# Kernel tuning notes

Hardware: AMD Instinct MI355X
Metric: run time of the kernel (lower is better)

## Reference

```python
import jax, jax.numpy as jnp
import numpy as np
from jax import lax

K = 10
ALPHA = 0.1
N_NODES = 100000
N_EDGES = 3200000


def setup_inputs() -> dict:
    key = jax.random.key(0)
    ks = jax.random.split(key, 6)
    x = jax.random.normal(ks[0], (N_NODES, 256), dtype=jnp.float32)
    edge_index = jax.random.randint(ks[1], (2, N_EDGES), 0, N_NODES, dtype=jnp.int64)
    w1 = jax.random.normal(ks[2], (256, 256), dtype=jnp.float32) * (1.0 / np.sqrt(256))
    b1 = jax.random.normal(ks[3], (256,), dtype=jnp.float32) * 0.01
    w2 = jax.random.normal(ks[4], (64, 256), dtype=jnp.float32) * (1.0 / np.sqrt(256))
    b2 = jax.random.normal(ks[5], (64,), dtype=jnp.float32) * 0.01
    return {"x": x, "edge_index": edge_index, "w1": w1, "b1": b1, "w2": w2, "b2": b2}


def reference(x, edge_index, w1, b1, w2, b2):
    # Eval mode: dropout is identity.
    h = jax.nn.relu(x @ w1.T + b1)          # [N, hidden]
    z = h @ w2.T + b2                        # [N, out]

    n = x.shape[0]
    loop = jnp.arange(n, dtype=edge_index.dtype)
    row = jnp.concatenate([edge_index[0], loop])   # sources (with self-loops)
    col = jnp.concatenate([edge_index[1], loop])   # targets (with self-loops)

    # gcn_norm: D^{-1/2} (A + I) D^{-1/2}, degree at target nodes
    deg = jax.ops.segment_sum(jnp.ones_like(col, dtype=z.dtype), col, num_segments=n)
    dinv = lax.rsqrt(deg)                    # deg >= 1 due to self-loops
    norm = dinv[row] * dinv[col]             # [E+N]

    x0 = z

    def step(xk, _):
        msg = xk[row] * norm[:, None]                          # gather + scale
        agg = jax.ops.segment_sum(msg, col, num_segments=n)    # scatter-add
        return (1.0 - ALPHA) * agg + ALPHA * x0, None

    out, _ = lax.scan(step, z, None, length=K)
    return out
```

## Files before the change

### kernel.cpp

```cpp
#include <hip/hip_runtime.h>
#include <hip/hip_bf16.h>


#define HIDDEN 256
#define OUTF   64
#define NB_BLK 256

typedef __attribute__((ext_vector_type(8))) unsigned short ushort8;
typedef __attribute__((ext_vector_type(8))) short short8v;
typedef __attribute__((ext_vector_type(4))) float f32x4;

__device__ inline float b2f(unsigned short u) {
    union { unsigned int i; float f; } c;
    c.i = ((unsigned int)u) << 16;
    return c.f;
}
__device__ inline unsigned short f2b(float f) {
    union { float f; unsigned int i; } c;
    c.f = f;
    unsigned int x = c.i;
    unsigned int r = (x + 0x7fff + ((x >> 16) & 1)) >> 16;
    return (unsigned short)r;
}
__device__ inline short8v cvt8v(float4 A, float4 B) {
    short8v o;
    o[0] = (short)f2b(A.x); o[1] = (short)f2b(A.y);
    o[2] = (short)f2b(A.z); o[3] = (short)f2b(A.w);
    o[4] = (short)f2b(B.x); o[5] = (short)f2b(B.y);
    o[6] = (short)f2b(B.z); o[7] = (short)f2b(B.w);
    return o;
}
__device__ inline short8v cvt8(const float* s) {
    return cvt8v(((const float4*)s)[0], ((const float4*)s)[1]);
}

__device__ inline bool detect_i64(const int* __restrict__ p) {
    int acc = 0;
#pragma unroll
    for (int i = 0; i < 16; ++i) acc |= p[2 * i + 1];
    return acc == 0;
}
__device__ inline int load_idx(const void* eiv, long long flat, bool is64) {
    if (is64) return (int)((const long long*)eiv)[flat];
    return ((const int*)eiv)[flat];
}

__global__ __launch_bounds__(256) void part_hist_kernel(const void* __restrict__ eiv,
                                                        long long E, int* __restrict__ bh,
                                                        int n, int nb) {
    __shared__ int hist[512];
    bool is64 = detect_i64((const int*)eiv);
    int t = threadIdx.x, b = blockIdx.x;
    for (int i = t; i < 512; i += 256) hist[i] = 0;
    __syncthreads();
    long long chunk = (E + NB_BLK - 1) / NB_BLK;
    long long beg = (long long)b * chunk, end = min(E, beg + chunk);
    for (long long e = beg + t; e < end; e += 256) {
        int c = load_idx(eiv, E + e, is64);
        if ((unsigned)c < (unsigned)n) atomicAdd(&hist[c >> 8], 1);
    }
    __syncthreads();
    for (int i = t; i < nb; i += 256) bh[i * NB_BLK + b] = hist[i];
}

__global__ __launch_bounds__(256) void part_colscan_kernel(const int* __restrict__ bh,
                                                           int* __restrict__ pre,
                                                           int* __restrict__ btot) {
    __shared__ int s[NB_BLK];
    int g = blockIdx.x, t = threadIdx.x;
    int v = bh[g * NB_BLK + t];
    s[t] = v;
    __syncthreads();
    for (int o = 1; o < NB_BLK; o <<= 1) {
        int tv = (t >= o) ? s[t - o] : 0;
        __syncthreads();
        s[t] += tv;
        __syncthreads();
    }
    pre[g * NB_BLK + t] = s[t] - v;
    if (t == NB_BLK - 1) btot[g] = s[t];
}

__global__ __launch_bounds__(512) void part_bscan_kernel(const int* __restrict__ btot,
                                                         int* __restrict__ bofs, int nb) {
    __shared__ int s[512];
    int t = threadIdx.x;
    int v = (t < nb) ? btot[t] : 0;
    s[t] = v;
    __syncthreads();
    for (int o = 1; o < 512; o <<= 1) {
        int tv = (t >= o) ? s[t - o] : 0;
        __syncthreads();
        s[t] += tv;
        __syncthreads();
    }
    if (t < nb) bofs[t] = s[t] - v;
    if (t == 511) bofs[nb] = s[511];
}

__global__ __launch_bounds__(256) void part_scatter_kernel(const void* __restrict__ eiv,
                                                           long long E,
                                                           const int* __restrict__ bofs,
                                                           const int* __restrict__ pre,
                                                           int2* __restrict__ pairs,
                                                           int n, int nb) {
    __shared__ int cur[512];
    bool is64 = detect_i64((const int*)eiv);
    int t = threadIdx.x, b = blockIdx.x;
    for (int i = t; i < nb; i += 256) cur[i] = bofs[i] + pre[i * NB_BLK + b];
    __syncthreads();
    long long chunk = (E + NB_BLK - 1) / NB_BLK;
    long long beg = (long long)b * chunk, end = min(E, beg + chunk);
    for (long long e = beg + t; e < end; e += 256) {
        int r = load_idx(eiv, e, is64);
        int c = load_idx(eiv, E + e, is64);
        if ((unsigned)c >= (unsigned)n || (unsigned)r >= (unsigned)n) continue;
        int pos = atomicAdd(&cur[c >> 8], 1);
        pairs[pos] = make_int2(c, r);
    }
}

__global__ __launch_bounds__(256) void csr_bucket_kernel(const int2* __restrict__ pairs,
                                                         const int* __restrict__ bofs,
                                                         int* __restrict__ ofs,
                                                         float* __restrict__ dinv,
                                                         int* __restrict__ csr_src,
                                                         int n, int nb) {
    __shared__ int hist[256];
    __shared__ int scn[256];
    int b = blockIdx.x;
    int t = threadIdx.x;
    int node0 = b << 8;
    int cnt = min(256, n - node0);

    hist[t] = 0;
    __syncthreads();
    int beg = bofs[b], end = bofs[b + 1];
    for (int e = beg + t; e < end; e += 256) atomicAdd(&hist[pairs[e].x & 255], 1);
    __syncthreads();
    int v = hist[t];
    scn[t] = v;
    __syncthreads();
    for (int o = 1; o < 256; o <<= 1) {
        int tv = (t >= o) ? scn[t - o] : 0;
        __syncthreads();
        scn[t] += tv;
        __syncthreads();
    }
    int excl = scn[t] - v;
    if (t < cnt) {
        ofs[node0 + t] = beg + excl;
        dinv[node0 + t] = rsqrtf((float)(v + 1));
    }
    if (b == nb - 1 && t == 0) ofs[n] = end;
    __syncthreads();
    hist[t] = beg + excl;
    __syncthreads();
    for (int e = beg + t; e < end; e += 256) {
        int2 p = pairs[e];
        int pos = atomicAdd(&hist[p.x & 255], 1);
        csr_src[pos] = p.y;
    }
}

__global__ __launch_bounds__(256) void pack_w_kernel(const float* __restrict__ w1,
                                                     const float* __restrict__ w2,
                                                     unsigned short* __restrict__ w1p,
                                                     unsigned short* __restrict__ w2p) {
    int id = blockIdx.x * 256 + threadIdx.x;
    if (id < 8192) {
        int ks = id >> 10, rem = id & 1023;
        int f = rem >> 2, kg = rem & 3;
        short8v o = cvt8(w1 + (size_t)f * HIDDEN + ks * 32 + kg * 8);
        *(short8v*)(w1p + ((size_t)(ks * 1024 + (f >> 4) * 64 + kg * 16 + (f & 15)) << 3)) = o;
    } else if (id < 8192 + 2048) {
        int q = id - 8192;
        int j = q >> 5, kslot = q & 31;
        short8v o = cvt8(w2 + (size_t)j * HIDDEN + kslot * 8);
        *(short8v*)(w2p +
                    ((size_t)((j >> 4) * 512 + (kslot >> 2) * 64 + (kslot & 3) * 16 + (j & 15))
                     << 3)) = o;
    }
}

__global__ __launch_bounds__(512) void mlp_mfma_kernel(const float* __restrict__ x,
                                                       const unsigned short* __restrict__ w1p,
                                                       const float* __restrict__ b1,
                                                       const unsigned short* __restrict__ w2p,
                                                       const float* __restrict__ b2,
                                                       const float* __restrict__ dinv,
                                                       unsigned short* __restrict__ xb0,
                                                       unsigned short* __restrict__ g0, int n) {
    __shared__ __align__(16) union {
        struct { unsigned short w1s[8192]; unsigned short xs[2048]; } p1;
        unsigned short h[64 * 264];
    } u;

    const int t = threadIdx.x;
    const int w = t >> 6;
    const int l = t & 63;
    const int c = l & 15, g = l >> 4;
    const int node0 = blockIdx.x * 64;

    const bool xrole = (t < 256);
    const int sm = t >> 2, skg = t & 3;
    const int snode = node0 + sm;
    const int wu0 = t - 256;
    const int xunit = ((sm >> 4) * 64 + skg * 16 + (sm & 15)) << 3;

    f32x4 acc[4][2];
#pragma unroll
    for (int a = 0; a < 4; ++a)
#pragma unroll
        for (int b = 0; b < 2; ++b) acc[a][b] = (f32x4)0.f;

    float4 pxa0 = make_float4(0.f, 0.f, 0.f, 0.f), pxb0 = pxa0;
    float4 pxa1 = pxa0, pxb1 = pxa0;
    short8v pw[4];

    auto loadx = [&](int ks, float4& A, float4& B) {
        if (snode < n) {
            const float4* xp = (const float4*)(x + (size_t)snode * HIDDEN + ks * 32 + skg * 8);
            A = xp[0];
            B = xp[1];
        }
    };
    auto loadw = [&](int ks) {
        const unsigned short* wsrc = w1p + (size_t)ks * 8192;
#pragma unroll
        for (int i = 0; i < 4; ++i)
            pw[i] = *(const short8v*)(wsrc + ((size_t)(wu0 + i * 256) << 3));
    };
    auto mfma_step = [&]() {
        short8v af[4], bf[2];
#pragma unroll
        for (int mt = 0; mt < 4; ++mt)
            af[mt] = *(const short8v*)&u.p1.xs[(mt * 64 + l) << 3];
#pragma unroll
        for (int j = 0; j < 2; ++j)
            bf[j] = *(const short8v*)&u.p1.w1s[((w * 2 + j) * 64 + l) << 3];
#pragma unroll
        for (int mt = 0; mt < 4; ++mt)
#pragma unroll
            for (int j = 0; j < 2; ++j)
                acc[mt][j] =
                    __builtin_amdgcn_mfma_f32_16x16x32_bf16(af[mt], bf[j], acc[mt][j], 0, 0, 0);
    };
    auto wwrite = [&]() {
#pragma unroll
        for (int i = 0; i < 4; ++i)
            *(short8v*)&u.p1.w1s[(wu0 + i * 256) << 3] = pw[i];
    };

    if (xrole) {
        loadx(0, pxa0, pxb0);
        loadx(1, pxa1, pxb1);
    } else {
        loadw(0);
    }

    for (int ks = 0; ks < 8; ks += 2) {
        if (xrole) *(short8v*)&u.p1.xs[xunit] = cvt8v(pxa0, pxb0);
        else wwrite();
        __syncthreads();
        if (xrole) {
            if (ks + 2 < 8) loadx(ks + 2, pxa0, pxb0);
        } else {
            loadw(ks + 1);
        }
        mfma_step();
        __syncthreads();
        if (xrole) *(short8v*)&u.p1.xs[xunit] = cvt8v(pxa1, pxb1);
        else wwrite();
        __syncthreads();
        if (xrole) {
            if (ks + 3 < 8) loadx(ks + 3, pxa1, pxb1);
        } else {
            if (ks + 2 < 8) loadw(ks + 2);
        }
        mfma_step();
        __syncthreads();
    }

#pragma unroll
    for (int j = 0; j < 2; ++j) {
        int col = w * 32 + j * 16 + c;
        float b1v = b1[col];
#pragma unroll
        for (int mt = 0; mt < 4; ++mt)
#pragma unroll
            for (int r = 0; r < 4; ++r) {
                int row = mt * 16 + g * 4 + r;
                u.h[row * 264 + col] = f2b(fmaxf(acc[mt][j][r] + b1v, 0.f));
            }
    }
    __syncthreads();

    const int rt = w >> 1;
    const int cb = (w & 1) * 2;
    f32x4 acc2[2];
#pragma unroll
    for (int j = 0; j < 2; ++j) acc2[j] = (f32x4)0.f;
#pragma unroll
    for (int ks = 0; ks < 8; ++ks) {
        short8v a2 = *(const short8v*)&u.h[(rt * 16 + c) * 264 + ks * 32 + g * 8];
#pragma unroll
        for (int j = 0; j < 2; ++j) {
            short8v bv = *(const short8v*)(w2p + ((size_t)((cb + j) * 512 + ks * 64 + l) << 3));
            acc2[j] = __builtin_amdgcn_mfma_f32_16x16x32_bf16(a2, bv, acc2[j], 0, 0, 0);
        }
    }
#pragma unroll
    for (int j = 0; j < 2; ++j) {
        int col = (cb + j) * 16 + c;
        float bb = b2[col];
#pragma unroll
        for (int r = 0; r < 4; ++r) {
            int node = node0 + rt * 16 + g * 4 + r;
            if (node < n) {
                float zv = acc2[j][r] + bb;
                float di = dinv[node];
                xb0[(size_t)node * OUTF + col] = f2b(0.1f * zv);
                g0[(size_t)node * OUTF + col] = f2b(di * zv);
            }
        }
    }
}

template <int LAST>
__global__ __launch_bounds__(256) void prop_kernel(const unsigned short* __restrict__ gk,
                                                   const unsigned short* __restrict__ xb0,
                                                   unsigned short* __restrict__ gn,
                                                   float* __restrict__ out,
                                                   const int* __restrict__ ofs,
                                                   const int* __restrict__ csr_src,
                                                   const float* __restrict__ dinv, int n) {
    int gid = blockIdx.x * 256 + threadIdx.x;
    int node = gid >> 5;
    int sub = gid & 31;
    int part = sub & 7;
    int q = sub >> 3;
    if (node >= n) return;

    int beg = ofs[node];
    int end = ofs[node + 1];
    int len = end - beg;
    int e0 = beg + ((len * q) >> 2);
    int e1 = beg + ((len * (q + 1)) >> 2);

    float acc[8];
#pragma unroll
    for (int j = 0; j < 8; ++j) acc[j] = 0.f;

    const size_t poff = (size_t)part * 8;
    int e = e0;
    for (; e + 3 < e1; e += 4) {
        int s0 = csr_src[e];
        int s1 = csr_src[e + 1];
        int s2 = csr_src[e + 2];
        int s3 = csr_src[e + 3];
        ushort8 a = *(const ushort8*)(gk + ((size_t)s0 << 6) + poff);
        ushort8 b = *(const ushort8*)(gk + ((size_t)s1 << 6) + poff);
        ushort8 cc = *(const ushort8*)(gk + ((size_t)s2 << 6) + poff);
        ushort8 d = *(const ushort8*)(gk + ((size_t)s3 << 6) + poff);
#pragma unroll
        for (int j = 0; j < 8; ++j) acc[j] += b2f(a[j]);
#pragma unroll
        for (int j = 0; j < 8; ++j) acc[j] += b2f(b[j]);
#pragma unroll
        for (int j = 0; j < 8; ++j) acc[j] += b2f(cc[j]);
#pragma unroll
        for (int j = 0; j < 8; ++j) acc[j] += b2f(d[j]);
    }
    for (; e < e1; ++e) {
        int s0 = csr_src[e];
        ushort8 a = *(const ushort8*)(gk + ((size_t)s0 << 6) + poff);
#pragma unroll
        for (int j = 0; j < 8; ++j) acc[j] += b2f(a[j]);
    }
    if (q == 0) {
        ushort8 a = *(const ushort8*)(gk + ((size_t)node << 6) + poff);
#pragma unroll
        for (int j = 0; j < 8; ++j) acc[j] += b2f(a[j]);
    }

#pragma unroll
    for (int j = 0; j < 8; ++j) acc[j] += __shfl_xor(acc[j], 8);
#pragma unroll
    for (int j = 0; j < 8; ++j) acc[j] += __shfl_xor(acc[j], 16);

    if (q != 0) return;

    float di = dinv[node];
    ushort8 xv = *(const ushort8*)(xb0 + ((size_t)node << 6) + poff);
    float res[8];
#pragma unroll
    for (int j = 0; j < 8; ++j) res[j] = 0.9f * di * acc[j] + b2f(xv[j]);

    if (LAST) {
        float4* o4 = (float4*)(out + (size_t)node * OUTF + poff);
        o4[0] = make_float4(res[0], res[1], res[2], res[3]);
        o4[1] = make_float4(res[4], res[5], res[6], res[7]);
    } else {
        ushort8 o;
#pragma unroll
        for (int j = 0; j < 8; ++j) o[j] = f2b(di * res[j]);
        *(ushort8*)(gn + ((size_t)node << 6) + poff) = o;
    }
}

extern "C" void kernel_launch(void* const* d_in, const int* in_sizes, int n_in,
                              void* d_out, int out_size, void* d_ws, size_t ws_size,
                              hipStream_t stream) {
    const float* x = (const float*)d_in[0];
    const void* ei = d_in[1];
    const float* w1 = (const float*)d_in[2];
    const float* b1 = (const float*)d_in[3];
    const float* w2 = (const float*)d_in[4];
    const float* b2 = (const float*)d_in[5];
    float* out = (float*)d_out;

    int n = in_sizes[0] / HIDDEN;
    long long E = (long long)in_sizes[1] / 2;
    int nb = (n + 255) >> 8;

    char* ws = (char*)d_ws;
    size_t off = 0;
    auto alloc = [&](size_t bytes) {
        void* p = ws + off;
        off += (bytes + 511) & ~(size_t)511;
        return p;
    };
    unsigned short* xb0 = (unsigned short*)alloc((size_t)n * OUTF * 2);
    size_t gmark = off;
    unsigned short* gA = (unsigned short*)alloc((size_t)n * OUTF * 2);
    unsigned short* gB = (unsigned short*)alloc((size_t)n * OUTF * 2);
    int2* pairs = (int2*)(ws + gmark);
    float* dinv = (float*)alloc((size_t)n * 4);
    int* ofs = (int*)alloc((size_t)(n + 1) * 4);
    int* csr_src = (int*)alloc((size_t)E * 4);
    int* bh = (int*)alloc((size_t)512 * NB_BLK * 4);
    int* pre = (int*)alloc((size_t)512 * NB_BLK * 4);
    int* btot = (int*)alloc(512 * 4);
    int* bofs = (int*)alloc(513 * 4);
    unsigned short* w1p = (unsigned short*)alloc(65536 * 2);
    unsigned short* w2p = (unsigned short*)alloc(16384 * 2);

    pack_w_kernel<<<40, 256, 0, stream>>>(w1, w2, w1p, w2p);

    part_hist_kernel<<<NB_BLK, 256, 0, stream>>>(ei, E, bh, n, nb);
    part_colscan_kernel<<<nb, NB_BLK, 0, stream>>>(bh, pre, btot);
    part_bscan_kernel<<<1, 512, 0, stream>>>(btot, bofs, nb);
    part_scatter_kernel<<<NB_BLK, 256, 0, stream>>>(ei, E, bofs, pre, pairs, n, nb);
    csr_bucket_kernel<<<nb, 256, 0, stream>>>(pairs, bofs, ofs, dinv, csr_src, n, nb);

    mlp_mfma_kernel<<<(n + 63) / 64, 512, 0, stream>>>(x, w1p, b1, w2p, b2, dinv, xb0, gA, n);

    int prop_blocks = (int)(((size_t)n * 32 + 255) / 256);
    for (int k = 0; k < 10; ++k) {
        const unsigned short* gin = (k & 1) ? gB : gA;
        unsigned short* gout = (k & 1) ? gA : gB;
        if (k == 9) {
            prop_kernel<1><<<prop_blocks, 256, 0, stream>>>(gin, xb0, nullptr, out, ofs,
                                                            csr_src, dinv, n);
        } else {
            prop_kernel<0><<<prop_blocks, 256, 0, stream>>>(gin, xb0, gout, nullptr, ofs,
                                                            csr_src, dinv, n);
        }
    }
}
```

Before: 681.4 us.

## Split features into two halves per XCD with dynamic chunk scheduling in propagation

```diff
diff --git a/kernel.cpp b/kernel.cpp
--- a/kernel.cpp
+++ b/kernel.cpp
@@ -102,7 +102,7 @@
                                                            long long E,
                                                            const int* __restrict__ bofs,
                                                            const int* __restrict__ pre,
-                                                           int2* __restrict__ pairs,
+                                                           unsigned int* __restrict__ pairs,
                                                            int n, int nb) {
     __shared__ int cur[512];
     bool is64 = detect_i64((const int*)eiv);
@@ -116,11 +116,11 @@
         int c = load_idx(eiv, E + e, is64);
         if ((unsigned)c >= (unsigned)n || (unsigned)r >= (unsigned)n) continue;
         int pos = atomicAdd(&cur[c >> 8], 1);
-        pairs[pos] = make_int2(c, r);
-    }
-}
-
-__global__ __launch_bounds__(256) void csr_bucket_kernel(const int2* __restrict__ pairs,
+        pairs[pos] = ((unsigned int)(c & 255) << 24) | (unsigned int)r;
+    }
+}
+
+__global__ __launch_bounds__(256) void csr_bucket_kernel(const unsigned int* __restrict__ pairs,
                                                          const int* __restrict__ bofs,
                                                          int* __restrict__ ofs,
                                                          float* __restrict__ dinv,
@@ -136,7 +136,7 @@
     hist[t] = 0;
     __syncthreads();
     int beg = bofs[b], end = bofs[b + 1];
-    for (int e = beg + t; e < end; e += 256) atomicAdd(&hist[pairs[e].x & 255], 1);
+    for (int e = beg + t; e < end; e += 256) atomicAdd(&hist[pairs[e] >> 24], 1);
     __syncthreads();
     int v = hist[t];
     scn[t] = v;
@@ -157,9 +157,9 @@
     hist[t] = beg + excl;
     __syncthreads();
     for (int e = beg + t; e < end; e += 256) {
-        int2 p = pairs[e];
-        int pos = atomicAdd(&hist[p.x & 255], 1);
-        csr_src[pos] = p.y;
+        unsigned int pr = pairs[e];
+        int pos = atomicAdd(&hist[pr >> 24], 1);
+        csr_src[pos] = (int)(pr & 0xFFFFFFu);
     }
 }
 
@@ -189,8 +189,10 @@
                                                        const unsigned short* __restrict__ w2p,
                                                        const float* __restrict__ b2,
                                                        const float* __restrict__ dinv,
-                                                       unsigned short* __restrict__ xb0,
-                                                       unsigned short* __restrict__ g0, int n) {
+                                                       unsigned short* __restrict__ xbh0,
+                                                       unsigned short* __restrict__ xbh1,
+                                                       unsigned short* __restrict__ g00,
+                                                       unsigned short* __restrict__ g01, int n) {
     __shared__ __align__(16) union {
         struct { unsigned short w1s[8192]; unsigned short xs[2048]; } p1;
         unsigned short h[64 * 264];
@@ -313,99 +315,111 @@
 #pragma unroll
     for (int j = 0; j < 2; ++j) {
         int col = (cb + j) * 16 + c;
+        int h2 = col >> 5;
+        int col32 = col & 31;
         float bb = b2[col];
+        unsigned short* xbp = h2 ? xbh1 : xbh0;
+        unsigned short* gp = h2 ? g01 : g00;
 #pragma unroll
         for (int r = 0; r < 4; ++r) {
             int node = node0 + rt * 16 + g * 4 + r;
             if (node < n) {
                 float zv = acc2[j][r] + bb;
                 float di = dinv[node];
-                xb0[(size_t)node * OUTF + col] = f2b(0.1f * zv);
-                g0[(size_t)node * OUTF + col] = f2b(di * zv);
+                size_t idx = ((size_t)node << 5) + col32;
+                xbp[idx] = f2b(0.1f * zv);
+                gp[idx] = f2b(di * zv);
             }
         }
     }
 }
 
 template <int LAST>
-__global__ __launch_bounds__(256) void prop_kernel(const unsigned short* __restrict__ gk,
-                                                   const unsigned short* __restrict__ xb0,
-                                                   unsigned short* __restrict__ gn,
+__global__ __launch_bounds__(256) void prop_kernel(const unsigned short* __restrict__ gi0,
+                                                   const unsigned short* __restrict__ gi1,
+                                                   const unsigned short* __restrict__ xbh0,
+                                                   const unsigned short* __restrict__ xbh1,
+                                                   unsigned short* __restrict__ go0,
+                                                   unsigned short* __restrict__ go1,
                                                    float* __restrict__ out,
                                                    const int* __restrict__ ofs,
                                                    const int* __restrict__ csr_src,
-                                                   const float* __restrict__ dinv, int n) {
-    int gid = blockIdx.x * 256 + threadIdx.x;
-    int node = gid >> 5;
-    int sub = gid & 31;
-    int part = sub & 7;
-    int q = sub >> 3;
-    if (node >= n) return;
-
-    int beg = ofs[node];
-    int end = ofs[node + 1];
-    int len = end - beg;
-    int e0 = beg + ((len * q) >> 2);
-    int e1 = beg + ((len * (q + 1)) >> 2);
-
-    float acc[8];
-#pragma unroll
-    for (int j = 0; j < 8; ++j) acc[j] = 0.f;
-
-    const size_t poff = (size_t)part * 8;
-    int e = e0;
-    for (; e + 3 < e1; e += 4) {
-        int s0 = csr_src[e];
-        int s1 = csr_src[e + 1];
-        int s2 = csr_src[e + 2];
-        int s3 = csr_src[e + 3];
-        ushort8 a = *(const ushort8*)(gk + ((size_t)s0 << 6) + poff);
-        ushort8 b = *(const ushort8*)(gk + ((size_t)s1 << 6) + poff);
-        ushort8 cc = *(const ushort8*)(gk + ((size_t)s2 << 6) + poff);
-        ushort8 d = *(const ushort8*)(gk + ((size_t)s3 << 6) + poff);
-#pragma unroll
-        for (int j = 0; j < 8; ++j) acc[j] += b2f(a[j]);
-#pragma unroll
-        for (int j = 0; j < 8; ++j) acc[j] += b2f(b[j]);
-#pragma unroll
-        for (int j = 0; j < 8; ++j) acc[j] += b2f(cc[j]);
-#pragma unroll
-        for (int j = 0; j < 8; ++j) acc[j] += b2f(d[j]);
-    }
-    for (; e < e1; ++e) {
-        int s0 = csr_src[e];
-        ushort8 a = *(const ushort8*)(gk + ((size_t)s0 << 6) + poff);
-#pragma unroll
-        for (int j = 0; j < 8; ++j) acc[j] += b2f(a[j]);
-    }
-    if (q == 0) {
-        ushort8 a = *(const ushort8*)(gk + ((size_t)node << 6) + poff);
-#pragma unroll
-        for (int j = 0; j < 8; ++j) acc[j] += b2f(a[j]);
-    }
-
-#pragma unroll
-    for (int j = 0; j < 8; ++j) acc[j] += __shfl_xor(acc[j], 8);
-#pragma unroll
-    for (int j = 0; j < 8; ++j) acc[j] += __shfl_xor(acc[j], 16);
-
-    if (q != 0) return;
-
-    float di = dinv[node];
-    ushort8 xv = *(const ushort8*)(xb0 + ((size_t)node << 6) + poff);
-    float res[8];
-#pragma unroll
-    for (int j = 0; j < 8; ++j) res[j] = 0.9f * di * acc[j] + b2f(xv[j]);
-
-    if (LAST) {
-        float4* o4 = (float4*)(out + (size_t)node * OUTF + poff);
-        o4[0] = make_float4(res[0], res[1], res[2], res[3]);
-        o4[1] = make_float4(res[4], res[5], res[6], res[7]);
-    } else {
-        ushort8 o;
-#pragma unroll
-        for (int j = 0; j < 8; ++j) o[j] = f2b(di * res[j]);
-        *(ushort8*)(gn + ((size_t)node << 6) + poff) = o;
+                                                   const float* __restrict__ dinv,
+                                                   int* __restrict__ cnt, int n) {
+    __shared__ int sc;
+    unsigned int xcd;
+    asm("s_getreg_b32 %0, hwreg(HW_REG_XCC_ID)" : "=s"(xcd));
+    const int t = threadIdx.x;
+    const int p = t & 3;
+    const int nl = t >> 2;
+    const int nchunks = (n + 63) >> 6;
+    const size_t poff = (size_t)p * 8;
+
+    for (int pass = 0; pass < 2; ++pass) {
+        const int h = ((int)xcd & 1) ^ pass;
+        const unsigned short* gi = h ? gi1 : gi0;
+        const unsigned short* xbh = h ? xbh1 : xbh0;
+        unsigned short* go = h ? go1 : go0;
+        for (;;) {
+            if (t == 0) sc = atomicAdd(&cnt[h], 1);
+            __syncthreads();
+            int chunk = sc;
+            __syncthreads();
+            if (chunk >= nchunks) break;
+            int node = (chunk << 6) + nl;
+            if (node < n) {
+                int beg = ofs[node];
+                int end = ofs[node + 1];
+                float acc[8];
+#pragma unroll
+                for (int j = 0; j < 8; ++j) acc[j] = 0.f;
+                int e = beg;
+                for (; e + 3 < end; e += 4) {
+                    int s0 = csr_src[e];
+                    int s1 = csr_src[e + 1];
+                    int s2 = csr_src[e + 2];
+                    int s3 = csr_src[e + 3];
+                    ushort8 a = *(const ushort8*)(gi + ((size_t)s0 << 5) + poff);
+                    ushort8 b = *(const ushort8*)(gi + ((size_t)s1 << 5) + poff);
+                    ushort8 cc = *(const ushort8*)(gi + ((size_t)s2 << 5) + poff);
+                    ushort8 d = *(const ushort8*)(gi + ((size_t)s3 << 5) + poff);
+#pragma unroll
+                    for (int j = 0; j < 8; ++j) acc[j] += b2f(a[j]);
+#pragma unroll
+                    for (int j = 0; j < 8; ++j) acc[j] += b2f(b[j]);
+#pragma unroll
+                    for (int j = 0; j < 8; ++j) acc[j] += b2f(cc[j]);
+#pragma unroll
+                    for (int j = 0; j < 8; ++j) acc[j] += b2f(d[j]);
+                }
+                for (; e < end; ++e) {
+                    int s0 = csr_src[e];
+                    ushort8 a = *(const ushort8*)(gi + ((size_t)s0 << 5) + poff);
+#pragma unroll
+                    for (int j = 0; j < 8; ++j) acc[j] += b2f(a[j]);
+                }
+                {
+                    ushort8 a = *(const ushort8*)(gi + ((size_t)node << 5) + poff);
+#pragma unroll
+                    for (int j = 0; j < 8; ++j) acc[j] += b2f(a[j]);
+                }
+                float di = dinv[node];
+                ushort8 xv = *(const ushort8*)(xbh + ((size_t)node << 5) + poff);
+                float res[8];
+#pragma unroll
+                for (int j = 0; j < 8; ++j) res[j] = 0.9f * di * acc[j] + b2f(xv[j]);
+                if (LAST) {
+                    float4* o4 = (float4*)(out + (size_t)node * OUTF + ((size_t)h << 5) + poff);
+                    o4[0] = make_float4(res[0], res[1], res[2], res[3]);
+                    o4[1] = make_float4(res[4], res[5], res[6], res[7]);
+                } else {
+                    ushort8 o;
+#pragma unroll
+                    for (int j = 0; j < 8; ++j) o[j] = f2b(di * res[j]);
+                    *(ushort8*)(go + ((size_t)node << 5) + poff) = o;
+                }
+            }
+        }
     }
 }
 
@@ -431,11 +445,15 @@
         off += (bytes + 511) & ~(size_t)511;
         return p;
     };
-    unsigned short* xb0 = (unsigned short*)alloc((size_t)n * OUTF * 2);
+    size_t HBYTES = (size_t)n * 32 * 2;
+    unsigned short* xbh0 = (unsigned short*)alloc(HBYTES);
+    unsigned short* xbh1 = (unsigned short*)alloc(HBYTES);
     size_t gmark = off;
-    unsigned short* gA = (unsigned short*)alloc((size_t)n * OUTF * 2);
-    unsigned short* gB = (unsigned short*)alloc((size_t)n * OUTF * 2);
-    int2* pairs = (int2*)(ws + gmark);
+    unsigned short* gA0 = (unsigned short*)alloc(HBYTES);
+    unsigned short* gA1 = (unsigned short*)alloc(HBYTES);
+    unsigned short* gB0 = (unsigned short*)alloc(HBYTES);
+    unsigned short* gB1 = (unsigned short*)alloc(HBYTES);
+    unsigned int* pairs = (unsigned int*)(ws + gmark);
     float* dinv = (float*)alloc((size_t)n * 4);
     int* ofs = (int*)alloc((size_t)(n + 1) * 4);
     int* csr_src = (int*)alloc((size_t)E * 4);
@@ -445,6 +463,9 @@
     int* bofs = (int*)alloc(513 * 4);
     unsigned short* w1p = (unsigned short*)alloc(65536 * 2);
     unsigned short* w2p = (unsigned short*)alloc(16384 * 2);
+    int* cnt = (int*)alloc(32 * 4);
+
+    hipMemsetAsync(cnt, 0, 32 * 4, stream);
 
     pack_w_kernel<<<40, 256, 0, stream>>>(w1, w2, w1p, w2p);
 
@@ -454,18 +475,23 @@
     part_scatter_kernel<<<NB_BLK, 256, 0, stream>>>(ei, E, bofs, pre, pairs, n, nb);
     csr_bucket_kernel<<<nb, 256, 0, stream>>>(pairs, bofs, ofs, dinv, csr_src, n, nb);
 
-    mlp_mfma_kernel<<<(n + 63) / 64, 512, 0, stream>>>(x, w1p, b1, w2p, b2, dinv, xb0, gA, n);
-
-    int prop_blocks = (int)(((size_t)n * 32 + 255) / 256);
+    mlp_mfma_kernel<<<(n + 63) / 64, 512, 0, stream>>>(x, w1p, b1, w2p, b2, dinv, xbh0, xbh1,
+                                                       gA0, gA1, n);
+
+    const int PROP_BLOCKS = 2048;
     for (int k = 0; k < 10; ++k) {
-        const unsigned short* gin = (k & 1) ? gB : gA;
-        unsigned short* gout = (k & 1) ? gA : gB;
+        const unsigned short* gi0 = (k & 1) ? gB0 : gA0;
+        const unsigned short* gi1 = (k & 1) ? gB1 : gA1;
+        unsigned short* go0 = (k & 1) ? gA0 : gB0;
+        unsigned short* go1 = (k & 1) ? gA1 : gB1;
         if (k == 9) {
-            prop_kernel<1><<<prop_blocks, 256, 0, stream>>>(gin, xb0, nullptr, out, ofs,
-                                                            csr_src, dinv, n);
+            prop_kernel<1><<<PROP_BLOCKS, 256, 0, stream>>>(gi0, gi1, xbh0, xbh1, nullptr,
+                                                            nullptr, out, ofs, csr_src, dinv,
+                                                            cnt + k * 2, n);
         } else {
-            prop_kernel<0><<<prop_blocks, 256, 0, stream>>>(gin, xb0, gout, nullptr, ofs,
-                                                            csr_src, dinv, n);
-        }
-    }
-}
+            prop_kernel<0><<<PROP_BLOCKS, 256, 0, stream>>>(gi0, gi1, xbh0, xbh1, go0, go1,
+                                                            nullptr, ofs, csr_src, dinv,
+                                                            cnt + k * 2, n);
+        }
+    }
+}
```

Measured after the change: 1.512 ms. +121.9%, slower.

## Use one 8-thread group per node in propagation and pack edge pairs into 32 bits

Applied to the files above, without the earlier changes.

```diff
diff --git a/kernel.cpp b/kernel.cpp
--- a/kernel.cpp
+++ b/kernel.cpp
@@ -102,7 +102,7 @@
                                                            long long E,
                                                            const int* __restrict__ bofs,
                                                            const int* __restrict__ pre,
-                                                           int2* __restrict__ pairs,
+                                                           unsigned int* __restrict__ pairs,
                                                            int n, int nb) {
     __shared__ int cur[512];
     bool is64 = detect_i64((const int*)eiv);
@@ -116,11 +116,11 @@
         int c = load_idx(eiv, E + e, is64);
         if ((unsigned)c >= (unsigned)n || (unsigned)r >= (unsigned)n) continue;
         int pos = atomicAdd(&cur[c >> 8], 1);
-        pairs[pos] = make_int2(c, r);
-    }
-}
-
-__global__ __launch_bounds__(256) void csr_bucket_kernel(const int2* __restrict__ pairs,
+        pairs[pos] = ((unsigned int)(c & 255) << 24) | (unsigned int)r;
+    }
+}
+
+__global__ __launch_bounds__(256) void csr_bucket_kernel(const unsigned int* __restrict__ pairs,
                                                          const int* __restrict__ bofs,
                                                          int* __restrict__ ofs,
                                                          float* __restrict__ dinv,
@@ -136,7 +136,7 @@
     hist[t] = 0;
     __syncthreads();
     int beg = bofs[b], end = bofs[b + 1];
-    for (int e = beg + t; e < end; e += 256) atomicAdd(&hist[pairs[e].x & 255], 1);
+    for (int e = beg + t; e < end; e += 256) atomicAdd(&hist[pairs[e] >> 24], 1);
     __syncthreads();
     int v = hist[t];
     scn[t] = v;
@@ -157,9 +157,9 @@
     hist[t] = beg + excl;
     __syncthreads();
     for (int e = beg + t; e < end; e += 256) {
-        int2 p = pairs[e];
-        int pos = atomicAdd(&hist[p.x & 255], 1);
-        csr_src[pos] = p.y;
+        unsigned int pr = pairs[e];
+        int pos = atomicAdd(&hist[pr >> 24], 1);
+        csr_src[pos] = (int)(pr & 0xFFFFFFu);
     }
 }
 
@@ -328,33 +328,29 @@
 }
 
 template <int LAST>
-__global__ __launch_bounds__(256) void prop_kernel(const unsigned short* __restrict__ gk,
-                                                   const unsigned short* __restrict__ xb0,
-                                                   unsigned short* __restrict__ gn,
-                                                   float* __restrict__ out,
-                                                   const int* __restrict__ ofs,
-                                                   const int* __restrict__ csr_src,
-                                                   const float* __restrict__ dinv, int n) {
+__global__ __launch_bounds__(256, 8) void prop_kernel(const unsigned short* __restrict__ gk,
+                                                      const unsigned short* __restrict__ xb0,
+                                                      unsigned short* __restrict__ gn,
+                                                      float* __restrict__ out,
+                                                      const int* __restrict__ ofs,
+                                                      const int* __restrict__ csr_src,
+                                                      const float* __restrict__ dinv, int n) {
     int gid = blockIdx.x * 256 + threadIdx.x;
-    int node = gid >> 5;
-    int sub = gid & 31;
-    int part = sub & 7;
-    int q = sub >> 3;
+    int node = gid >> 3;
+    int part = gid & 7;
     if (node >= n) return;
 
     int beg = ofs[node];
     int end = ofs[node + 1];
-    int len = end - beg;
-    int e0 = beg + ((len * q) >> 2);
-    int e1 = beg + ((len * (q + 1)) >> 2);
+    float di = dinv[node];
 
     float acc[8];
 #pragma unroll
     for (int j = 0; j < 8; ++j) acc[j] = 0.f;
 
     const size_t poff = (size_t)part * 8;
-    int e = e0;
-    for (; e + 3 < e1; e += 4) {
+    int e = beg;
+    for (; e + 3 < end; e += 4) {
         int s0 = csr_src[e];
         int s1 = csr_src[e + 1];
         int s2 = csr_src[e + 2];
@@ -372,26 +368,18 @@
 #pragma unroll
         for (int j = 0; j < 8; ++j) acc[j] += b2f(d[j]);
     }
-    for (; e < e1; ++e) {
+    for (; e < end; ++e) {
         int s0 = csr_src[e];
         ushort8 a = *(const ushort8*)(gk + ((size_t)s0 << 6) + poff);
 #pragma unroll
         for (int j = 0; j < 8; ++j) acc[j] += b2f(a[j]);
     }
-    if (q == 0) {
+    {
         ushort8 a = *(const ushort8*)(gk + ((size_t)node << 6) + poff);
 #pragma unroll
         for (int j = 0; j < 8; ++j) acc[j] += b2f(a[j]);
     }
 
-#pragma unroll
-    for (int j = 0; j < 8; ++j) acc[j] += __shfl_xor(acc[j], 8);
-#pragma unroll
-    for (int j = 0; j < 8; ++j) acc[j] += __shfl_xor(acc[j], 16);
-
-    if (q != 0) return;
-
-    float di = dinv[node];
     ushort8 xv = *(const ushort8*)(xb0 + ((size_t)node << 6) + poff);
     float res[8];
 #pragma unroll
@@ -435,7 +423,7 @@
     size_t gmark = off;
     unsigned short* gA = (unsigned short*)alloc((size_t)n * OUTF * 2);
     unsigned short* gB = (unsigned short*)alloc((size_t)n * OUTF * 2);
-    int2* pairs = (int2*)(ws + gmark);
+    unsigned int* pairs = (unsigned int*)(ws + gmark);
     float* dinv = (float*)alloc((size_t)n * 4);
     int* ofs = (int*)alloc((size_t)(n + 1) * 4);
     int* csr_src = (int*)alloc((size_t)E * 4);
@@ -456,7 +444,7 @@
 
     mlp_mfma_kernel<<<(n + 63) / 64, 512, 0, stream>>>(x, w1p, b1, w2p, b2, dinv, xb0, gA, n);
 
-    int prop_blocks = (int)(((size_t)n * 32 + 255) / 256);
+    int prop_blocks = (int)(((size_t)n * 8 + 255) / 256);
     for (int k = 0; k < 10; ++k) {
         const unsigned short* gin = (k & 1) ? gB : gA;
         unsigned short* gout = (k & 1) ? gA : gB;
```

New measurement: 684.2 us. No clear change (+0.4%).
